# Optimization experiments

Measured on AMD Instinct MI355X. Metric: run time of the kernel, lower is better.

The kernel has to match this reference:

```python
import jax, jax.numpy as jnp
import numpy as np

T, B, D = 200, 1024, 128
T_OBS = 140
L = 20       # rec_dims: encoder latent per mean/std
LAT = 32     # latents: generative latent dim
GRU_U = 200  # gru_units
UNITS = 100  # hidden units of ODE-func / z0 nets


def _lin(key, fan_in, fan_out):
    return jax.random.normal(key, (fan_in, fan_out), jnp.float32) / jnp.sqrt(jnp.float32(fan_in))


def setup_inputs() -> dict:
    key = jax.random.key(0)
    ks = jax.random.split(key, 20)
    gin = 2 * L + 2 * D  # GRU input: (mean,std) + (data,mask)
    inp = {
        "truth": jax.random.normal(ks[0], (T, B, D), jnp.float32),
        "t": jnp.arange(T, dtype=jnp.float32),
        "obs_idx": jnp.sort(jax.random.randint(ks[1], (T_OBS,), 0, T)),
        "eps": jax.random.normal(ks[2], (B, LAT), jnp.float32),
        # encoder ODE func (rec_layers=1 hidden layer of UNITS)
        "enc_w1": _lin(ks[3], L, UNITS), "enc_b1": jnp.zeros(UNITS, jnp.float32),
        "enc_w2": _lin(ks[4], UNITS, L), "enc_b2": jnp.zeros(L, jnp.float32),
        # GRU unit: update / reset / new-state nets
        "gru_uw1": _lin(ks[5], gin, GRU_U), "gru_ub1": jnp.zeros(GRU_U, jnp.float32),
        "gru_uw2": _lin(ks[6], GRU_U, 2 * L), "gru_ub2": jnp.zeros(2 * L, jnp.float32),
        "gru_rw1": _lin(ks[7], gin, GRU_U), "gru_rb1": jnp.zeros(GRU_U, jnp.float32),
        "gru_rw2": _lin(ks[8], GRU_U, 2 * L), "gru_rb2": jnp.zeros(2 * L, jnp.float32),
        "gru_nw1": _lin(ks[9], gin, GRU_U), "gru_nb1": jnp.zeros(GRU_U, jnp.float32),
        "gru_nw2": _lin(ks[10], GRU_U, 2 * L), "gru_nb2": jnp.zeros(2 * L, jnp.float32),
        # transform hidden -> z0 (mean,std)
        "z0_w1": _lin(ks[11], 2 * L, UNITS), "z0_b1": jnp.zeros(UNITS, jnp.float32),
        "z0_w2": _lin(ks[12], UNITS, 2 * LAT), "z0_b2": jnp.zeros(2 * LAT, jnp.float32),
        # decoder ODE func (gen_layers=2 hidden layers of UNITS)
        "dec_w1": _lin(ks[13], LAT, UNITS), "dec_b1": jnp.zeros(UNITS, jnp.float32),
        "dec_w2": _lin(ks[14], UNITS, UNITS), "dec_b2": jnp.zeros(UNITS, jnp.float32),
        "dec_w3": _lin(ks[15], UNITS, LAT), "dec_b3": jnp.zeros(LAT, jnp.float32),
        # readout latent -> data space
        "out_w": _lin(ks[16], LAT, D), "out_b": jnp.zeros(D, jnp.float32),
    }
    return inp


def _rk4(f, y, dt):
    k1 = f(y)
    k2 = f(y + 0.5 * dt * k1)
    k3 = f(y + 0.5 * dt * k2)
    k4 = f(y + dt * k3)
    return y + (dt / 6.0) * (k1 + 2.0 * k2 + 2.0 * k3 + k4)


def reference(truth, t, obs_idx, eps,
              enc_w1, enc_b1, enc_w2, enc_b2,
              gru_uw1, gru_ub1, gru_uw2, gru_ub2,
              gru_rw1, gru_rb1, gru_rw2, gru_rb2,
              gru_nw1, gru_nb1, gru_nw2, gru_nb2,
              z0_w1, z0_b1, z0_w2, z0_b2,
              dec_w1, dec_b1, dec_w2, dec_b2, dec_w3, dec_b3,
              out_w, out_b):
    enc_f = lambda y: jnp.tanh(y @ enc_w1 + enc_b1) @ enc_w2 + enc_b2
    dec_f = lambda z: (jnp.tanh(jnp.tanh(z @ dec_w1 + dec_b1) @ dec_w2 + dec_b2)
                       @ dec_w3 + dec_b3)

    # ----- ODE-RNN encoder, run_backwards=True over observed timesteps -----
    x_obs = truth[obs_idx][::-1]                     # [To, B, D], time-reversed
    t_obs = t[obs_idx][::-1]
    dts = jnp.concatenate([jnp.zeros(1, t.dtype), jnp.diff(t_obs)])  # <=0 steps

    def enc_step(carry, inp):
        ym, ys = carry                               # [B,L] each
        x, dt = inp
        ym = _rk4(enc_f, ym, dt)                     # evolve mean between obs
        xm = jnp.concatenate([x, jnp.ones_like(x)], -1)   # data + mask(=1)
        y = jnp.concatenate([ym, ys], -1)            # [B, 2L]
        yc = jnp.concatenate([y, xm], -1)            # [B, 2L+2D]
        u = jax.nn.sigmoid(jnp.tanh(yc @ gru_uw1 + gru_ub1) @ gru_uw2 + gru_ub2)
        r = jax.nn.sigmoid(jnp.tanh(yc @ gru_rw1 + gru_rb1) @ gru_rw2 + gru_rb2)
        nc = jnp.concatenate([y * r, xm], -1)
        ns = jnp.tanh(nc @ gru_nw1 + gru_nb1) @ gru_nw2 + gru_nb2
        nm, nsd = ns[:, :L], jnp.abs(ns[:, L:])
        new_y = (1.0 - u) * jnp.concatenate([nm, nsd], -1) + u * y
        return (new_y[:, :L], new_y[:, L:]), None

    nb = truth.shape[1]
    init = (jnp.zeros((nb, L), truth.dtype), jnp.zeros((nb, L), truth.dtype))
    (ym, ys), _ = jax.lax.scan(enc_step, init, (x_obs, dts))

    # ----- z0 posterior and sample (n_traj_samples=1) -----
    h = jnp.tanh(jnp.concatenate([ym, ys], -1) @ z0_w1 + z0_b1) @ z0_w2 + z0_b2
    z0_mean, z0_std = h[:, :LAT], jnp.abs(h[:, LAT:])
    z = z0_mean + eps * z0_std                       # [B, LAT]

    # ----- Neural ODE decoder over time_steps_to_predict = t -----
    def dec_step(zc, dt):
        zn = _rk4(dec_f, zc, dt)
        return zn, zn
    _, zs = jax.lax.scan(dec_step, z, jnp.diff(t))
    sol = jnp.concatenate([z[None], zs], 0)          # [T, B, LAT]

    out = sol @ out_w + out_b                        # [T, B, D]
    return jnp.transpose(out, (1, 0, 2))[None]       # [1, B, T, D]
```

## Files before the change

kernel.cpp:

```cpp
#include <hip/hip_runtime.h>
#include <math.h>

#define BB 1024
#define DD 128
#define NWG 256
#define CH 28
#define NCH 5

#define WS_WPACK 0
#define WS_B1E   81920
#define WS_W1Y   82560
#define WS_Y     106560
#define WS_Z     147520
#define WS_HPRE  180288
#define WS_SOL   180288

__device__ __forceinline__ float bcast(float v, int lane) {
    return __uint_as_float(__builtin_amdgcn_readlane(__float_as_uint(v), lane));
}

__global__ __launch_bounds__(256) void prep_kernel(
    const float* __restrict__ uw1, const float* __restrict__ ub1,
    const float* __restrict__ rw1, const float* __restrict__ rb1,
    const float* __restrict__ nw1, const float* __restrict__ nb1,
    float* __restrict__ ws)
{
    int tid = blockIdx.x * blockDim.x + threadIdx.x;
    int nth = gridDim.x * blockDim.x;
    for (int idx = tid; idx < 128 * 640; idx += nth) {
        int k = idx / 640, j = idx - k * 640;
        float v = 0.f;
        if (j < 600) {
            int g = j / 200, jj = j - g * 200;
            const float* w1 = (g == 0) ? uw1 : (g == 1) ? rw1 : nw1;
            v = w1[(40 + k) * 200 + jj];
        }
        ws[WS_WPACK + idx] = v;
    }
    for (int j = tid; j < 640; j += nth) {
        float s = 0.f;
        if (j < 600) {
            int g = j / 200, jj = j - g * 200;
            const float* w1 = (g == 0) ? uw1 : (g == 1) ? rw1 : nw1;
            const float* b1 = (g == 0) ? ub1 : (g == 1) ? rb1 : nb1;
            s = b1[jj];
            for (int k = 168; k < 296; ++k) s += w1[k * 200 + jj];
        }
        ws[WS_B1E + j] = s;
    }
    for (int idx = tid; idx < 40 * 600; idx += nth) {
        int k = idx / 600, j = idx - k * 600;
        int g = j / 200, jj = j - g * 200;
        const float* w1 = (g == 0) ? uw1 : (g == 1) ? rw1 : nw1;
        ws[WS_W1Y + idx] = w1[k * 200 + jj];
    }
}

__global__ __launch_bounds__(256) void hpre_gemm(
    const float* __restrict__ truth, const int* __restrict__ obs_idx,
    const float* __restrict__ ws, float* __restrict__ hpre, int s0)
{
    __shared__ float sx[64][68];
    __shared__ float sw[64][132];
    const int t0 = threadIdx.x;
    const int jt = blockIdx.x % 5;
    const int bt = (blockIdx.x / 5) % 16;
    const int sl = blockIdx.x / 80;
    const int oi = obs_idx[139 - (s0 + sl)];
    const int b0 = bt * 64;
    const float* wpack = ws + WS_WPACK;
    const float* b1e   = ws + WS_B1E;

    const int jj  = t0 & 15;
    const int bb4 = t0 >> 4;
    float acc[8][4];
#pragma unroll
    for (int m = 0; m < 8; ++m)
#pragma unroll
        for (int q = 0; q < 4; ++q) acc[m][q] = 0.f;

    for (int kh = 0; kh < 2; ++kh) {
        __syncthreads();
        for (int i = t0; i < 64 * 16; i += 256) {
            int bb = i >> 4, kq = i & 15;
            const float4 v = *(const float4*)&truth[((size_t)oi * BB + b0 + bb) * DD + kh * 64 + kq * 4];
            *(float4*)&sx[bb][kq * 4] = v;
        }
        for (int i = t0; i < 64 * 32; i += 256) {
            int kk = i >> 5, jq = i & 31;
            const float4 v = *(const float4*)&wpack[(kh * 64 + kk) * 640 + jt * 128 + jq * 4];
            *(float4*)&sw[kk][jq * 4] = v;
        }
        __syncthreads();
#pragma unroll 4
        for (int k = 0; k < 64; ++k) {
            float xv[4], wv[8];
#pragma unroll
            for (int q = 0; q < 4; ++q) xv[q] = sx[bb4 * 4 + q][k];
#pragma unroll
            for (int m = 0; m < 8; ++m) wv[m] = sw[k][jj + 16 * m];
#pragma unroll
            for (int m = 0; m < 8; ++m)
#pragma unroll
                for (int q = 0; q < 4; ++q) acc[m][q] += wv[m] * xv[q];
        }
    }
    const int bblk = bt * 16 + bb4;
#pragma unroll
    for (int m = 0; m < 8; ++m) {
        int j = jt * 128 + jj + 16 * m;
        if (j < 600) {
            float be = b1e[j];
#pragma unroll
            for (int q = 0; q < 4; ++q)
                hpre[(size_t)((sl * 256 + bblk) * 4 + q) * 600 + j] = acc[m][q] + be;
        }
    }
}

__global__ __launch_bounds__(256, 1) void enc_chunk(
    const float* __restrict__ tg, const int* __restrict__ obs_idx,
    const float* __restrict__ eps,
    const float* __restrict__ ew1, const float* __restrict__ eb1,
    const float* __restrict__ ew2, const float* __restrict__ eb2,
    const float* __restrict__ uw2, const float* __restrict__ ub2,
    const float* __restrict__ rw2, const float* __restrict__ rb2,
    const float* __restrict__ nw2, const float* __restrict__ nb2,
    const float* __restrict__ z0w1, const float* __restrict__ z0b1,
    const float* __restrict__ z0w2, const float* __restrict__ z0b2,
    float* __restrict__ ws, int s0)
{
    __shared__ float s_t[200];
    __shared__ int   s_oi[140];
    __shared__ __align__(16) float s_y[40][4];
    __shared__ __align__(16) float s_ytmp[20][4];
    __shared__ float s_kacc[20][4];
    __shared__ __align__(16) float s_hid[4][104];
    __shared__ float s_pe[20][4][2];
    __shared__ __align__(16) float s_ew1t[100 * 20];
    __shared__ __align__(16) float s_w2n[40 * 212];
    __shared__ __align__(16) float s_hur[4][416];
    __shared__ __align__(16) float s_hn[4][208];
    __shared__ float s_pw[80][4][4];
    __shared__ float s_pn[40][4][4];
    __shared__ float s_u[40][4];
    __shared__ __align__(16) float s_yr[40][4];
    __shared__ float s_z0o[4][64];

    const int t0 = threadIdx.x;
    const int bblk = blockIdx.x;
    const int b0 = bblk * 4;
    const float* hpre = ws + WS_HPRE;

    float rgy[3][40];
    float rew2h[52];
    float rw2q[2][52];
    float eb1_r = 0.f, eb2_r = 0.f, bur_r = 0.f, bn_r = 0.f;

    if (t0 < 200) {
#pragma unroll
        for (int g = 0; g < 3; ++g)
#pragma unroll
            for (int k = 0; k < 40; ++k)
                rgy[g][k] = ws[WS_W1Y + k * 600 + g * 200 + t0];
    }
    if (t0 < 100) eb1_r = eb1[t0];
    if (t0 < 160) {
        const int c2 = t0 % 20, kh = t0 / 80;
#pragma unroll
        for (int i = 0; i < 52; ++i) {
            const int row = kh * 52 + i;
            rew2h[i] = (row < 100) ? ew2[row * 20 + c2] : 0.f;
        }
    }
    if (t0 < 80) eb2_r = eb2[t0 % 20];
    if (t0 < 160) {
        const int p = t0 % 20, g = (t0 / 20) % 2, kq = t0 / 40;
        const float* w2 = g ? rw2 : uw2;
#pragma unroll
        for (int j = 0; j < 2; ++j)
#pragma unroll
            for (int i = 0; i < 52; ++i) {
                const int row = kq * 52 + i;
                rw2q[j][i] = (row < 200) ? w2[row * 40 + p + 20 * j] : 0.f;
            }
        bur_r = ((t0 % 80) < 40) ? ub2[t0 % 80] : rb2[(t0 % 80) - 40];
        bn_r = nb2[t0 % 40];
    }

    for (int i = t0; i < 2000; i += 256) { int k = i / 100, c = i % 100; s_ew1t[c * 20 + k] = ew1[i]; }
    for (int i = t0; i < 40 * 212; i += 256) { int o = i / 212, k = i % 212; s_w2n[i] = (k < 200) ? nw2[k * 40 + o] : 0.f; }
    for (int i = t0; i < 200; i += 256) s_t[i] = tg[i];
    for (int i = t0; i < 140; i += 256) s_oi[i] = obs_idx[i];
    if (t0 < 160) { int k = t0 % 40, b = t0 / 40; s_y[k][b] = s0 ? ws[WS_Y + k * 1024 + b0 + b] : 0.f; }
    if (t0 < 4) {
#pragma unroll
        for (int i = 0; i < 4; ++i) s_hid[t0][100 + i] = 0.f;
#pragma unroll
        for (int i = 0; i < 8; ++i) { s_hur[t0][200 + i] = 0.f; s_hur[t0][408 + i] = 0.f; s_hn[t0][200 + i] = 0.f; }
    }
    __syncthreads();

    for (int sl = 0; sl < CH; ++sl) {
        const int s = s0 + sl;
        const int oi = s_oi[139 - s];
        const float dt = (s == 0) ? 0.f : (s_t[oi] - s_t[s_oi[140 - s]]);

        float hpu[4], hpr[4], hpn[4];
        if (t0 < 200) {
#pragma unroll
            for (int q = 0; q < 4; ++q) {
                const size_t r = (size_t)((sl * 256 + bblk) * 4 + q) * 600;
                hpu[q] = hpre[r + t0];
                hpr[q] = hpre[r + 200 + t0];
                hpn[q] = hpre[r + 400 + t0];
            }
        }

#pragma unroll 1
        for (int e = 0; e < 4; ++e) {
            if (t0 < 100) {
                const int c = t0;
                float a[4] = {eb1_r, eb1_r, eb1_r, eb1_r};
#pragma unroll
                for (int i = 0; i < 5; ++i) {
                    const float4 wv = *(const float4*)&s_ew1t[c * 20 + 4 * i];
                    const float wk[4] = {wv.x, wv.y, wv.z, wv.w};
#pragma unroll
                    for (int kk = 0; kk < 4; ++kk) {
                        const int k = 4 * i + kk;
                        const float4 yv = (e == 0) ? *(const float4*)&s_y[k][0]
                                                   : *(const float4*)&s_ytmp[k][0];
                        a[0] += wk[kk] * yv.x; a[1] += wk[kk] * yv.y;
                        a[2] += wk[kk] * yv.z; a[3] += wk[kk] * yv.w;
                    }
                }
#pragma unroll
                for (int b = 0; b < 4; ++b) s_hid[b][c] = tanhf(a[b]);
            }
            __syncthreads();
            if (t0 < 160) {
                const int c2 = t0 % 20, b = (t0 / 20) % 4, kh = t0 / 80;
                float acc = 0.f;
#pragma unroll
                for (int i = 0; i < 13; ++i) {
                    const float4 hv = *(const float4*)&s_hid[b][kh * 52 + 4 * i];
                    acc += hv.x * rew2h[4 * i] + hv.y * rew2h[4 * i + 1]
                         + hv.z * rew2h[4 * i + 2] + hv.w * rew2h[4 * i + 3];
                }
                s_pe[c2][b][kh] = acc;
            }
            __syncthreads();
            if (t0 < 80) {
                const int c2 = t0 % 20, b = t0 / 20;
                const float kv = eb2_r + s_pe[c2][b][0] + s_pe[c2][b][1];
                const float y0 = s_y[c2][b];
                if (e == 0)      { s_kacc[c2][b] = kv;        s_ytmp[c2][b] = y0 + 0.5f * dt * kv; }
                else if (e == 1) { s_kacc[c2][b] += 2.f * kv; s_ytmp[c2][b] = y0 + 0.5f * dt * kv; }
                else if (e == 2) { s_kacc[c2][b] += 2.f * kv; s_ytmp[c2][b] = y0 + dt * kv; }
                else             { s_y[c2][b] = y0 + (dt / 6.f) * (s_kacc[c2][b] + kv); }
            }
            __syncthreads();
        }

        if (t0 < 200) {
            float au[4], ar[4];
#pragma unroll
            for (int b = 0; b < 4; ++b) { au[b] = hpu[b]; ar[b] = hpr[b]; }
#pragma unroll
            for (int k = 0; k < 40; ++k) {
                const float4 yv = *(const float4*)&s_y[k][0];
                const float wu = rgy[0][k], wr = rgy[1][k];
                au[0] += wu * yv.x; au[1] += wu * yv.y; au[2] += wu * yv.z; au[3] += wu * yv.w;
                ar[0] += wr * yv.x; ar[1] += wr * yv.y; ar[2] += wr * yv.z; ar[3] += wr * yv.w;
            }
#pragma unroll
            for (int b = 0; b < 4; ++b) {
                s_hur[b][t0] = tanhf(au[b]);
                s_hur[b][208 + t0] = tanhf(ar[b]);
            }
        }
        __syncthreads();

        if (t0 < 160) {
            const int p = t0 % 20, g = (t0 / 20) % 2, kq = t0 / 40;
            const int goff = g * 208;
            float a1[4] = {0.f, 0.f, 0.f, 0.f}, a2[4] = {0.f, 0.f, 0.f, 0.f};
#pragma unroll
            for (int i = 0; i < 13; ++i) {
                const float wa = rw2q[0][4 * i], wb = rw2q[0][4 * i + 1],
                            wc = rw2q[0][4 * i + 2], wd = rw2q[0][4 * i + 3];
                const float we = rw2q[1][4 * i], wf = rw2q[1][4 * i + 1],
                            wg = rw2q[1][4 * i + 2], wh = rw2q[1][4 * i + 3];
#pragma unroll
                for (int b = 0; b < 4; ++b) {
                    const float4 hv = *(const float4*)&s_hur[b][goff + kq * 52 + 4 * i];
                    a1[b] += hv.x * wa + hv.y * wb + hv.z * wc + hv.w * wd;
                    a2[b] += hv.x * we + hv.y * wf + hv.z * wg + hv.w * wh;
                }
            }
            const int o1 = 40 * g + p, o2 = o1 + 20;
#pragma unroll
            for (int b = 0; b < 4; ++b) { s_pw[o1][b][kq] = a1[b]; s_pw[o2][b][kq] = a2[b]; }
        }
        __syncthreads();

        if (t0 < 160) {
            const int o = t0 % 80, bp = t0 / 80;
#pragma unroll
            for (int j = 0; j < 2; ++j) {
                const int b = 2 * bp + j;
                const float v = bur_r + s_pw[o][b][0] + s_pw[o][b][1] + s_pw[o][b][2] + s_pw[o][b][3];
                const float sg = 1.f / (1.f + expf(-v));
                if (o < 40) s_u[o][b] = sg;
                else        s_yr[o - 40][b] = s_y[o - 40][b] * sg;
            }
        }
        __syncthreads();

        if (t0 < 200) {
            float an[4];
#pragma unroll
            for (int b = 0; b < 4; ++b) an[b] = hpn[b];
#pragma unroll
            for (int k = 0; k < 40; ++k) {
                const float4 yv = *(const float4*)&s_yr[k][0];
                const float w = rgy[2][k];
                an[0] += w * yv.x; an[1] += w * yv.y; an[2] += w * yv.z; an[3] += w * yv.w;
            }
#pragma unroll
            for (int b = 0; b < 4; ++b) s_hn[b][t0] = tanhf(an[b]);
        }
        __syncthreads();

        if (t0 < 160) {
            const int o = t0 % 40, kq = t0 / 40;
            float an[4] = {0.f, 0.f, 0.f, 0.f};
#pragma unroll
            for (int i = 0; i < 13; ++i) {
                const float4 wv = *(const float4*)&s_w2n[o * 212 + kq * 52 + 4 * i];
#pragma unroll
                for (int b = 0; b < 4; ++b) {
                    const float4 hv = *(const float4*)&s_hn[b][kq * 52 + 4 * i];
                    an[b] += hv.x * wv.x + hv.y * wv.y + hv.z * wv.z + hv.w * wv.w;
                }
            }
#pragma unroll
            for (int b = 0; b < 4; ++b) s_pn[o][b][kq] = an[b];
        }
        __syncthreads();

        if (t0 < 160) {
            const int o = t0 % 40, b = t0 / 40;
            const float v = bn_r + s_pn[o][b][0] + s_pn[o][b][1] + s_pn[o][b][2] + s_pn[o][b][3];
            const float cand = (o < 20) ? v : fabsf(v);
            const float uu = s_u[o][b];
            s_y[o][b] = (1.f - uu) * cand + uu * s_y[o][b];
        }
        __syncthreads();
    }

    if (s0 + CH == 140) {
        if (t0 < 100) {
            const int c = t0;
            float a[4] = {z0b1[c], z0b1[c], z0b1[c], z0b1[c]};
#pragma unroll
            for (int k = 0; k < 40; ++k) {
                const float4 yv = *(const float4*)&s_y[k][0];
                const float w = z0w1[k * 100 + c];
                a[0] += w * yv.x; a[1] += w * yv.y; a[2] += w * yv.z; a[3] += w * yv.w;
            }
#pragma unroll
            for (int b = 0; b < 4; ++b) s_hid[b][c] = tanhf(a[b]);
        }
        __syncthreads();
        {
            const int b = t0 / 64, u = t0 % 64;
            float acc = z0b2[u];
#pragma unroll
            for (int i = 0; i < 25; ++i) {
                const float4 hv = *(const float4*)&s_hid[b][4 * i];
                acc += hv.x * z0w2[(4 * i) * 64 + u] + hv.y * z0w2[(4 * i + 1) * 64 + u]
                     + hv.z * z0w2[(4 * i + 2) * 64 + u] + hv.w * z0w2[(4 * i + 3) * 64 + u];
            }
            s_z0o[b][u] = acc;
        }
        __syncthreads();
        if (t0 < 128) {
            const int b = t0 / 32, i = t0 % 32;
            const int gb = b0 + b;
            ws[WS_Z + gb * 32 + i] = s_z0o[b][i] + eps[gb * 32 + i] * fabsf(s_z0o[b][32 + i]);
        }
    }
    if (t0 < 160) {
        const int k = t0 % 40, b = t0 / 40;
        ws[WS_Y + k * 1024 + b0 + b] = s_y[k][b];
    }
}

__global__ __launch_bounds__(256, 1) void dec_kernel(
    const float* __restrict__ tg,
    const float* __restrict__ dw1, const float* __restrict__ db1,
    const float* __restrict__ dw2, const float* __restrict__ db2,
    const float* __restrict__ dw3, const float* __restrict__ db3,
    float* __restrict__ ws)
{
    __shared__ float s_t[200];

    const int t0 = threadIdx.x;
    const int w  = t0 >> 6;
    const int l  = t0 & 63;
    const int batch = blockIdx.x * 4 + w;

    const int c0 = l;
    const int c1 = 64 + l;
    const bool has1 = (c1 < 100);
    const int j3 = l & 31;

    float rw1a[32], rw1b[32], rw2a[100], rw2b[100], rw3[100];
#pragma unroll
    for (int k = 0; k < 32; ++k) {
        rw1a[k] = dw1[k * 100 + c0];
        rw1b[k] = has1 ? dw1[k * 100 + c1] : 0.f;
    }
#pragma unroll
    for (int k = 0; k < 100; ++k) {
        rw2a[k] = dw2[k * 100 + c0];
        rw2b[k] = has1 ? dw2[k * 100 + c1] : 0.f;
        rw3[k]  = dw3[k * 32 + j3];
    }
    const float rb1a = db1[c0];
    const float rb1b = has1 ? db1[c1] : 0.f;
    const float rb2a = db2[c0];
    const float rb2b = has1 ? db2[c1] : 0.f;
    const float rb3  = db3[j3];

    for (int i = t0; i < 200; i += 256) s_t[i] = tg[i];

    float z_r = 0.f;
    if (l < 32) z_r = ws[WS_Z + (size_t)batch * 32 + l];
    __syncthreads();

    float zs = z_r;
    float ka_r = 0.f;

    for (int s = 0; s < 200; ++s) {
        if (l < 32)
            ws[WS_SOL + (size_t)(s * 1024 + batch) * 32 + l] = z_r;
        if (s == 199) break;
        const float dtv = s_t[s + 1] - s_t[s];

#pragma unroll 1
        for (int e = 0; e < 4; ++e) {
            float a0 = rb1a, a1 = rb1b;
#pragma unroll
            for (int k = 0; k < 32; ++k) {
                const float sv = bcast(zs, k);
                a0 += sv * rw1a[k];
                a1 += sv * rw1b[k];
            }
            const float h1_0 = tanhf(a0);
            const float h1_1 = tanhf(a1);

            float a2 = rb2a, a3 = rb2b;
#pragma unroll
            for (int k = 0; k < 64; ++k) {
                const float sv = bcast(h1_0, k);
                a2 += sv * rw2a[k];
                a3 += sv * rw2b[k];
            }
#pragma unroll
            for (int k = 0; k < 36; ++k) {
                const float sv = bcast(h1_1, k);
                a2 += sv * rw2a[64 + k];
                a3 += sv * rw2b[64 + k];
            }
            const float h2_0 = tanhf(a2);
            const float h2_1 = tanhf(a3);

            float ak = rb3;
#pragma unroll
            for (int k = 0; k < 64; ++k) ak += bcast(h2_0, k) * rw3[k];
#pragma unroll
            for (int k = 0; k < 36; ++k) ak += bcast(h2_1, k) * rw3[64 + k];

            if (e == 0)      { ka_r = ak;        zs = z_r + 0.5f * dtv * ak; }
            else if (e == 1) { ka_r += 2.f * ak; zs = z_r + 0.5f * dtv * ak; }
            else if (e == 2) { ka_r += 2.f * ak; zs = z_r + dtv * ak; }
            else             { z_r += (dtv / 6.f) * (ka_r + ak); zs = z_r; }
        }
    }
}

__global__ __launch_bounds__(256) void proj_kernel(
    const float* __restrict__ ow, const float* __restrict__ ob,
    const float* __restrict__ ws, float* __restrict__ out)
{
    const int t0 = threadIdx.x;
    const int d = t0 & 127, half = t0 >> 7;
    float rw[32];
#pragma unroll
    for (int k = 0; k < 32; ++k) rw[k] = ow[k * 128 + d];
    const float bo = ob[d];
    const int sb0 = blockIdx.x * 64 + half * 32;
#pragma unroll 2
    for (int m = 0; m < 32; ++m) {
        const int sb = sb0 + m;
        const int s = sb >> 10, b = sb & 1023;
        const float4* zp = (const float4*)&ws[WS_SOL + (size_t)sb * 32];
        float acc = bo;
#pragma unroll
        for (int kq = 0; kq < 8; ++kq) {
            const float4 zv = zp[kq];
            acc += zv.x * rw[4 * kq] + zv.y * rw[4 * kq + 1]
                 + zv.z * rw[4 * kq + 2] + zv.w * rw[4 * kq + 3];
        }
        out[((size_t)b * 200 + s) * 128 + d] = acc;
    }
}

extern "C" void kernel_launch(void* const* d_in, const int* in_sizes, int n_in,
                              void* d_out, int out_size, void* d_ws, size_t ws_size,
                              hipStream_t stream)
{
    const float* truth = (const float*)d_in[0];
    const float* tg    = (const float*)d_in[1];
    const int*   oi    = (const int*)d_in[2];
    const float* eps   = (const float*)d_in[3];
    const float* ew1   = (const float*)d_in[4];
    const float* eb1   = (const float*)d_in[5];
    const float* ew2   = (const float*)d_in[6];
    const float* eb2   = (const float*)d_in[7];
    const float* uw1   = (const float*)d_in[8];
    const float* ub1   = (const float*)d_in[9];
    const float* uw2   = (const float*)d_in[10];
    const float* ub2   = (const float*)d_in[11];
    const float* rw1   = (const float*)d_in[12];
    const float* rb1   = (const float*)d_in[13];
    const float* rw2   = (const float*)d_in[14];
    const float* rb2   = (const float*)d_in[15];
    const float* nw1   = (const float*)d_in[16];
    const float* nb1   = (const float*)d_in[17];
    const float* nw2   = (const float*)d_in[18];
    const float* nb2   = (const float*)d_in[19];
    const float* z0w1  = (const float*)d_in[20];
    const float* z0b1  = (const float*)d_in[21];
    const float* z0w2  = (const float*)d_in[22];
    const float* z0b2  = (const float*)d_in[23];
    const float* dw1   = (const float*)d_in[24];
    const float* db1   = (const float*)d_in[25];
    const float* dw2   = (const float*)d_in[26];
    const float* db2   = (const float*)d_in[27];
    const float* dw3   = (const float*)d_in[28];
    const float* db3   = (const float*)d_in[29];
    const float* ow    = (const float*)d_in[30];
    const float* ob    = (const float*)d_in[31];
    float* ws  = (float*)d_ws;
    float* out = (float*)d_out;

    prep_kernel<<<dim3(120), dim3(256), 0, stream>>>(uw1, ub1, rw1, rb1, nw1, nb1, ws);
    for (int c = 0; c < NCH; ++c) {
        hpre_gemm<<<dim3(CH * 16 * 5), dim3(256), 0, stream>>>(truth, oi, ws, ws + WS_HPRE, c * CH);
        enc_chunk<<<dim3(NWG), dim3(256), 0, stream>>>(
            tg, oi, eps, ew1, eb1, ew2, eb2, uw2, ub2, rw2, rb2, nw2, nb2,
            z0w1, z0b1, z0w2, z0b2, ws, c * CH);
    }
    dec_kernel<<<dim3(256), dim3(256), 0, stream>>>(tg, dw1, db1, dw2, db2, dw3, db3, ws);
    proj_kernel<<<dim3(3200), dim3(256), 0, stream>>>(ow, ob, ws, out);
}
```

Measured before the change: 4.424 ms.

## Split decoder ODE MLP across two wavefronts per batch element with fast tanh

Measured after the change: 4.102 ms. 1.08x faster.

```diff
diff --git a/kernel.cpp b/kernel.cpp
--- a/kernel.cpp
+++ b/kernel.cpp
@@ -17,6 +17,11 @@
 
 __device__ __forceinline__ float bcast(float v, int lane) {
     return __uint_as_float(__builtin_amdgcn_readlane(__float_as_uint(v), lane));
+}
+
+__device__ __forceinline__ float tanh_fast(float x) {
+    const float t = __builtin_amdgcn_exp2f(x * 2.88539008177793f);
+    return 1.f - 2.f * __builtin_amdgcn_rcpf(t + 1.f);
 }
 
 __global__ __launch_bounds__(256) void prep_kernel(
@@ -398,7 +403,7 @@
     }
 }
 
-__global__ __launch_bounds__(256, 1) void dec_kernel(
+__global__ __launch_bounds__(128, 2) void dec_kernel(
     const float* __restrict__ tg,
     const float* __restrict__ dw1, const float* __restrict__ db1,
     const float* __restrict__ dw2, const float* __restrict__ db2,
@@ -406,28 +411,31 @@
     float* __restrict__ ws)
 {
     __shared__ float s_t[200];
+    __shared__ float s_p1[2][100];
+    __shared__ float s_p2[2][100];
+    __shared__ float s_p3[2][32];
 
     const int t0 = threadIdx.x;
     const int w  = t0 >> 6;
     const int l  = t0 & 63;
-    const int batch = blockIdx.x * 4 + w;
+    const int batch = blockIdx.x;
 
     const int c0 = l;
     const int c1 = 64 + l;
-    const bool has1 = (c1 < 100);
+    const bool has1 = (l < 36);
     const int j3 = l & 31;
 
-    float rw1a[32], rw1b[32], rw2a[100], rw2b[100], rw3[100];
-#pragma unroll
-    for (int k = 0; k < 32; ++k) {
-        rw1a[k] = dw1[k * 100 + c0];
-        rw1b[k] = has1 ? dw1[k * 100 + c1] : 0.f;
-    }
-#pragma unroll
-    for (int k = 0; k < 100; ++k) {
-        rw2a[k] = dw2[k * 100 + c0];
-        rw2b[k] = has1 ? dw2[k * 100 + c1] : 0.f;
-        rw3[k]  = dw3[k * 32 + j3];
+    float rw1a[16], rw1b[16], rw2a[50], rw2b[50], rw3[50];
+#pragma unroll
+    for (int i = 0; i < 16; ++i) {
+        rw1a[i] = dw1[(16 * w + i) * 100 + c0];
+        rw1b[i] = has1 ? dw1[(16 * w + i) * 100 + c1] : 0.f;
+    }
+#pragma unroll
+    for (int i = 0; i < 50; ++i) {
+        rw2a[i] = dw2[(50 * w + i) * 100 + c0];
+        rw2b[i] = has1 ? dw2[(50 * w + i) * 100 + c1] : 0.f;
+        rw3[i]  = dw3[(50 * w + i) * 32 + j3];
     }
     const float rb1a = db1[c0];
     const float rb1b = has1 ? db1[c1] : 0.f;
@@ -435,59 +443,84 @@
     const float rb2b = has1 ? db2[c1] : 0.f;
     const float rb3  = db3[j3];
 
-    for (int i = t0; i < 200; i += 256) s_t[i] = tg[i];
-
-    float z_r = 0.f;
-    if (l < 32) z_r = ws[WS_Z + (size_t)batch * 32 + l];
+    for (int i = t0; i < 200; i += 128) s_t[i] = tg[i];
+
+    float z_r = ws[WS_Z + (size_t)batch * 32 + j3];
     __syncthreads();
 
-    float zs = z_r;
-    float ka_r = 0.f;
+    float zs = z_r, ka_r = 0.f;
 
     for (int s = 0; s < 200; ++s) {
-        if (l < 32)
+        if (t0 < 32)
             ws[WS_SOL + (size_t)(s * 1024 + batch) * 32 + l] = z_r;
         if (s == 199) break;
         const float dtv = s_t[s + 1] - s_t[s];
 
 #pragma unroll 1
         for (int e = 0; e < 4; ++e) {
-            float a0 = rb1a, a1 = rb1b;
-#pragma unroll
-            for (int k = 0; k < 32; ++k) {
-                const float sv = bcast(zs, k);
-                a0 += sv * rw1a[k];
-                a1 += sv * rw1b[k];
-            }
-            const float h1_0 = tanhf(a0);
-            const float h1_1 = tanhf(a1);
-
-            float a2 = rb2a, a3 = rb2b;
-#pragma unroll
-            for (int k = 0; k < 64; ++k) {
-                const float sv = bcast(h1_0, k);
-                a2 += sv * rw2a[k];
-                a3 += sv * rw2b[k];
-            }
-#pragma unroll
-            for (int k = 0; k < 36; ++k) {
-                const float sv = bcast(h1_1, k);
-                a2 += sv * rw2a[64 + k];
-                a3 += sv * rw2b[64 + k];
-            }
-            const float h2_0 = tanhf(a2);
-            const float h2_1 = tanhf(a3);
-
-            float ak = rb3;
-#pragma unroll
-            for (int k = 0; k < 64; ++k) ak += bcast(h2_0, k) * rw3[k];
-#pragma unroll
-            for (int k = 0; k < 36; ++k) ak += bcast(h2_1, k) * rw3[64 + k];
-
-            if (e == 0)      { ka_r = ak;        zs = z_r + 0.5f * dtv * ak; }
-            else if (e == 1) { ka_r += 2.f * ak; zs = z_r + 0.5f * dtv * ak; }
-            else if (e == 2) { ka_r += 2.f * ak; zs = z_r + dtv * ak; }
-            else             { z_r += (dtv / 6.f) * (ka_r + ak); zs = z_r; }
+            float a0 = 0.f, a1 = 0.f;
+            if (w == 0) {
+#pragma unroll
+                for (int i = 0; i < 16; ++i) {
+                    const float sv = bcast(zs, i);
+                    a0 += sv * rw1a[i]; a1 += sv * rw1b[i];
+                }
+            } else {
+#pragma unroll
+                for (int i = 0; i < 16; ++i) {
+                    const float sv = bcast(zs, 16 + i);
+                    a0 += sv * rw1a[i]; a1 += sv * rw1b[i];
+                }
+            }
+            s_p1[w][c0] = a0;
+            if (has1) s_p1[w][c1] = a1;
+            __syncthreads();
+            const float h1_0 = tanh_fast(rb1a + a0 + s_p1[w ^ 1][c0]);
+            const float h1_1 = has1 ? tanh_fast(rb1b + a1 + s_p1[w ^ 1][c1]) : 0.f;
+
+            float a2 = 0.f, a3 = 0.f;
+            if (w == 0) {
+#pragma unroll
+                for (int i = 0; i < 50; ++i) {
+                    const float sv = bcast(h1_0, i);
+                    a2 += sv * rw2a[i]; a3 += sv * rw2b[i];
+                }
+            } else {
+#pragma unroll
+                for (int i = 0; i < 14; ++i) {
+                    const float sv = bcast(h1_0, 50 + i);
+                    a2 += sv * rw2a[i]; a3 += sv * rw2b[i];
+                }
+#pragma unroll
+                for (int i = 14; i < 50; ++i) {
+                    const float sv = bcast(h1_1, i - 14);
+                    a2 += sv * rw2a[i]; a3 += sv * rw2b[i];
+                }
+            }
+            s_p2[w][c0] = a2;
+            if (has1) s_p2[w][c1] = a3;
+            __syncthreads();
+            const float h2_0 = tanh_fast(rb2a + a2 + s_p2[w ^ 1][c0]);
+            const float h2_1 = has1 ? tanh_fast(rb2b + a3 + s_p2[w ^ 1][c1]) : 0.f;
+
+            float ap = 0.f;
+            if (w == 0) {
+#pragma unroll
+                for (int i = 0; i < 50; ++i) ap += bcast(h2_0, i) * rw3[i];
+            } else {
+#pragma unroll
+                for (int i = 0; i < 14; ++i) ap += bcast(h2_0, 50 + i) * rw3[i];
+#pragma unroll
+                for (int i = 14; i < 50; ++i) ap += bcast(h2_1, i - 14) * rw3[i];
+            }
+            if (l < 32) s_p3[w][l] = ap;
+            __syncthreads();
+            const float kj = rb3 + s_p3[0][j3] + s_p3[1][j3];
+
+            if (e == 0)      { ka_r = kj;        zs = z_r + 0.5f * dtv * kj; }
+            else if (e == 1) { ka_r += 2.f * kj; zs = z_r + 0.5f * dtv * kj; }
+            else if (e == 2) { ka_r += 2.f * kj; zs = z_r + dtv * kj; }
+            else             { z_r += (dtv / 6.f) * (ka_r + kj); zs = z_r; }
         }
     }
 }
@@ -565,6 +598,6 @@
             tg, oi, eps, ew1, eb1, ew2, eb2, uw2, ub2, rw2, rb2, nw2, nb2,
             z0w1, z0b1, z0w2, z0b2, ws, c * CH);
     }
-    dec_kernel<<<dim3(256), dim3(256), 0, stream>>>(tg, dw1, db1, dw2, db2, dw3, db3, ws);
+    dec_kernel<<<dim3(1024), dim3(128), 0, stream>>>(tg, dw1, db1, dw2, db2, dw3, db3, ws);
     proj_kernel<<<dim3(3200), dim3(256), 0, stream>>>(ow, ob, ws, out);
 }
```
